# Performance work log

Measured on AMD Instinct MI355X. Metric: run time of the kernel, lower is better.

The kernel has to match this reference:

```python
import jax, jax.numpy as jnp
import numpy as np

N, L, H, Q = 64, 258, 1024, 256
WINDOW = 16.0
DEV_POW = 128.0  # 2 * (window/2)^2, Luong local-p sigma = D/2


def setup_inputs() -> dict:
    key = jax.random.key(0)
    k1, k2, k3, k4, k5, k6 = jax.random.split(key, 6)
    encoder_outputs = jax.random.normal(k1, (N, L, H), dtype=jnp.float32)
    decoder_h_t = jax.random.normal(k2, (N, Q, H), dtype=jnp.float32)
    src_len = jax.random.randint(k3, (N,), 32, L + 1).astype(jnp.int32)
    # window centers within each source sentence
    p_t = jax.random.uniform(k4, (N,), dtype=jnp.float32) * (src_len.astype(jnp.float32) - 1.0)
    W_a = jax.random.normal(k5, (H, H), dtype=jnp.float32) * (1.0 / np.sqrt(H))
    W_c = jax.random.normal(k6, (H, 2 * H), dtype=jnp.float32) * (1.0 / np.sqrt(2 * H))
    return {"encoder_outputs": encoder_outputs, "decoder_h_t": decoder_h_t,
            "src_len": src_len, "p_t": p_t, "W_a": W_a, "W_c": W_c}


def reference(encoder_outputs, decoder_h_t, src_len, p_t, W_a, W_c):
    n, l, h = encoder_outputs.shape
    idx = jnp.arange(l, dtype=jnp.float32)  # index_matrix, length == max_length == L

    # local_p window: [p_t - D, p_t + D], clamped to [0, src_len]
    src_end = src_len.astype(jnp.float32)
    attn_start = jnp.maximum(p_t - WINDOW, 0.0)          # [N]
    attn_end = jnp.minimum(p_t + WINDOW, src_end)        # [N]
    mask = (idx[None, :] < attn_start[:, None]) | (idx[None, :] > attn_end[:, None])  # [N,L]

    # Luong 'general' score: h_t^T W_a h_s -> [N,Q,L]
    score = jnp.einsum('nqh,hk,nlk->nql', decoder_h_t, W_a, encoder_outputs)

    score = jnp.where(mask[:, None, :], -1e9, score)
    align = jax.nn.softmax(score, axis=2)                 # [N,Q,L]

    # gaussian reweighting centered at p_t
    gauss = jnp.exp(-((idx[None, :] - p_t[:, None]) ** 2) / DEV_POW)  # [N,L]
    align = align * gauss[:, None, :]

    context = jnp.einsum('nql,nlh->nqh', align, encoder_outputs)      # [N,Q,H]
    cat = jnp.concatenate([context, decoder_h_t], axis=2)             # [N,Q,2H]
    return jnp.tanh(cat @ W_c.T)                                      # [N,Q,H]
```

## Files before the change

### kernel.cpp

```cpp
#include <hip/hip_runtime.h>
#include <hip/hip_bf16.h>
#include <cstdint>

#define DEVINL __device__ __forceinline__

typedef __attribute__((ext_vector_type(8))) short short8;
typedef __attribute__((ext_vector_type(4))) float f32x4;
typedef __attribute__((ext_vector_type(4))) unsigned short u16x4;

static constexpr int NB = 64, LL = 258, HH = 1024, QQ = 256;
static constexpr int WROWS = 33;
static constexpr int MU = 2176;
static constexpr int VTN = 4096;

static constexpr size_t OFF_META = 0;
static constexpr size_t SZ_WE   = (size_t)MU * HH * 2;
static constexpr size_t OFF_WEHI = 1024;
static constexpr size_t OFF_WELO = OFF_WEHI + SZ_WE;
static constexpr size_t OFF_WAHI = OFF_WELO + SZ_WE;
static constexpr size_t OFF_WALO = OFF_WAHI + (size_t)HH * HH * 2;
static constexpr size_t OFF_WCBF = OFF_WALO + (size_t)HH * HH * 2;
static constexpr size_t OFF_HBF  = OFF_WCBF + (size_t)HH * 2 * HH * 2;
static constexpr size_t OFF_U    = OFF_HBF + (size_t)NB * QQ * HH * 2;
static constexpr size_t OFF_UHI  = OFF_U;
static constexpr size_t OFF_ULO  = OFF_U + (size_t)MU * HH * 2;
static constexpr size_t OFF_PHL  = OFF_U + (size_t)MU * HH * 4;
static constexpr size_t OFF_VT   = OFF_PHL + (size_t)NB * QQ * 128 * 2;

DEVINL unsigned short f2bf(float x) {
    union { float f; uint32_t u; } v; v.f = x;
    uint32_t u = v.u;
    uint32_t r = (u + 0x7FFFu + ((u >> 16) & 1u)) >> 16;
    return (unsigned short)r;
}
DEVINL float bf2f(unsigned short b) {
    union { uint32_t u; float f; } v; v.u = ((uint32_t)b) << 16;
    return v.f;
}

template <typename T>
DEVINL void lds_load16(const T* g, T* l) {
    __builtin_amdgcn_global_load_lds(
        (const __attribute__((address_space(1))) void*)g,
        (__attribute__((address_space(3))) void*)l, 16, 0, 0);
}

DEVINL float fast_tanh(float x) {
    float e = __expf(2.0f * x);
    return 1.0f - 2.0f / (e + 1.0f);
}

DEVINL void window_of(float p, int sl, int& ls, int& lc) {
    float se = (float)sl;
    float s = fmaxf(p - 16.0f, 0.0f);
    float e = fminf(p + 16.0f, se);
    ls = (int)ceilf(s);
    int le = (int)floorf(e); if (le > LL - 1) le = LL - 1;
    lc = le - ls + 1;
    if (lc < 0) lc = 0;
    if (lc > WROWS) lc = WROWS;
}

__global__ __launch_bounds__(256) void k_prep(const float* __restrict__ enc,
                                              const float* __restrict__ pt,
                                              const int* __restrict__ slen,
                                              const float* __restrict__ Wa,
                                              const float* __restrict__ Wc,
                                              unsigned short* __restrict__ wehi,
                                              unsigned short* __restrict__ welo,
                                              unsigned short* __restrict__ wahi,
                                              unsigned short* __restrict__ walo,
                                              unsigned short* __restrict__ wcbf) {
    const int b = blockIdx.x, t = threadIdx.x;
    if (b < MU) {
        int r = b;
        const float* src = nullptr;
        bool valid = false;
        if (r < NB * WROWS) {
            int n = r / WROWS, li = r - n * WROWS;
            int ls, lc;
            window_of(pt[n], slen[n], ls, lc);
            if (li < lc) { valid = true; src = enc + ((size_t)n * LL + ls + li) * HH; }
        }
        f32x4 v;
        if (valid) v = ((const f32x4*)src)[t];
        else { v[0] = 0.f; v[1] = 0.f; v[2] = 0.f; v[3] = 0.f; }
        u16x4 h, l;
#pragma unroll
        for (int j = 0; j < 4; ++j) {
            unsigned short hb = f2bf(v[j]);
            h[j] = hb;
            l[j] = f2bf(v[j] - bf2f(hb));
        }
        size_t o = (size_t)r * HH / 4 + t;
        ((u16x4*)wehi)[o] = h;
        ((u16x4*)welo)[o] = l;
    } else if (b < MU + 1024) {
        int i = (b - MU) * 256 + t;
        f32x4 v = ((const f32x4*)Wa)[i];
        u16x4 h, l;
#pragma unroll
        for (int j = 0; j < 4; ++j) {
            unsigned short hb = f2bf(v[j]);
            h[j] = hb;
            l[j] = f2bf(v[j] - bf2f(hb));
        }
        ((u16x4*)wahi)[i] = h;
        ((u16x4*)walo)[i] = l;
    } else {
        int i = (b - MU - 1024) * 256 + t;
        f32x4 v = ((const f32x4*)Wc)[i];
        u16x4 h;
#pragma unroll
        for (int j = 0; j < 4; ++j) h[j] = f2bf(v[j]);
        ((u16x4*)wcbf)[i] = h;
    }
}

__global__ __launch_bounds__(256) void k_wgemm(const unsigned short* __restrict__ wehi,
                                               const unsigned short* __restrict__ welo,
                                               const unsigned short* __restrict__ wahi,
                                               const unsigned short* __restrict__ walo,
                                               const unsigned short* __restrict__ wcbf,
                                               unsigned short* __restrict__ Uhi,
                                               unsigned short* __restrict__ Ulo,
                                               unsigned short* __restrict__ VT) {
    __shared__ unsigned short smem[24576];
    const int tid = threadIdx.x;
    const int bid = blockIdx.x;

    const int w = tid >> 6, lane = tid & 63;
    const int wr = w >> 1, wc = w & 1;
    const int r16 = lane & 15, khalf = lane >> 4, rg = lane >> 4;
    const int srow = tid >> 2;
    const int scol = ((tid & 3) ^ ((tid >> 3) & 3)) * 8;
    const int kslot = (khalf ^ ((r16 >> 1) & 3)) * 8;

    if (bid < 272) {
        const int m0 = (bid >> 3) * 64;
        const int n0 = (bid & 7) * 128;
        f32x4 acc[2][4] = {};

        auto stage = [&](int buf, int kb) {
            lds_load16(wehi + (size_t)(m0 + srow) * HH + kb + scol, &smem[buf * 2048 + tid * 8]);
            lds_load16(welo + (size_t)(m0 + srow) * HH + kb + scol, &smem[4096 + buf * 2048 + tid * 8]);
#pragma unroll
            for (int i = 0; i < 2; ++i) {
                lds_load16(wahi + (size_t)(n0 + i * 64 + srow) * HH + kb + scol,
                           &smem[8192 + buf * 4096 + i * 2048 + tid * 8]);
                lds_load16(walo + (size_t)(n0 + i * 64 + srow) * HH + kb + scol,
                           &smem[16384 + buf * 4096 + i * 2048 + tid * 8]);
            }
        };

        stage(0, 0);
        for (int t = 0; t < 32; ++t) {
            const int buf = t & 1;
            asm volatile("s_waitcnt vmcnt(0)" ::: "memory");
            __builtin_amdgcn_s_barrier();
            short8 ah[2], al[2], bh[4], bl[4];
#pragma unroll
            for (int f = 0; f < 2; ++f) {
                int ai = buf * 2048 + (wr * 32 + f * 16 + r16) * 32 + kslot;
                ah[f] = *(const short8*)&smem[ai];
                al[f] = *(const short8*)&smem[4096 + ai];
            }
#pragma unroll
            for (int nf = 0; nf < 4; ++nf) {
                int bi = buf * 4096 + (wc * 64 + nf * 16 + r16) * 32 + kslot;
                bh[nf] = *(const short8*)&smem[8192 + bi];
                bl[nf] = *(const short8*)&smem[16384 + bi];
            }
            if (t + 1 < 32) stage(buf ^ 1, (t + 1) * 32);
            asm volatile("s_waitcnt lgkmcnt(0)" ::: "memory");
            __builtin_amdgcn_sched_barrier(0);
#pragma unroll
            for (int mf = 0; mf < 2; ++mf)
#pragma unroll
                for (int nf = 0; nf < 4; ++nf) {
                    acc[mf][nf] = __builtin_amdgcn_mfma_f32_16x16x32_bf16(ah[mf], bh[nf], acc[mf][nf], 0, 0, 0);
                    acc[mf][nf] = __builtin_amdgcn_mfma_f32_16x16x32_bf16(ah[mf], bl[nf], acc[mf][nf], 0, 0, 0);
                    acc[mf][nf] = __builtin_amdgcn_mfma_f32_16x16x32_bf16(al[mf], bh[nf], acc[mf][nf], 0, 0, 0);
                }
            __builtin_amdgcn_s_barrier();
        }
#pragma unroll
        for (int mf = 0; mf < 2; ++mf)
#pragma unroll
            for (int nf = 0; nf < 4; ++nf)
#pragma unroll
                for (int r = 0; r < 4; ++r) {
                    int m = m0 + wr * 32 + mf * 16 + rg * 4 + r;
                    int nn = n0 + wc * 64 + nf * 16 + r16;
                    float v = acc[mf][nf][r];
                    unsigned short h = f2bf(v);
                    Uhi[(size_t)m * HH + nn] = h;
                    Ulo[(size_t)m * HH + nn] = f2bf(v - bf2f(h));
                }
    } else {
        const int b2 = bid - 272;
        const int m0 = (b2 / 17) * 64;
        const int n0 = (b2 % 17) * 128;
        f32x4 acc[2][4] = {};

        auto stage = [&](int buf, int kb) {
            lds_load16(wcbf + (size_t)(m0 + srow) * (2 * HH) + kb + scol, &smem[buf * 2048 + tid * 8]);
#pragma unroll
            for (int i = 0; i < 2; ++i) {
                lds_load16(wehi + (size_t)(n0 + i * 64 + srow) * HH + kb + scol,
                           &smem[8192 + buf * 4096 + i * 2048 + tid * 8]);
                lds_load16(welo + (size_t)(n0 + i * 64 + srow) * HH + kb + scol,
                           &smem[16384 + buf * 4096 + i * 2048 + tid * 8]);
            }
        };

        stage(0, 0);
        for (int t = 0; t < 32; ++t) {
            const int buf = t & 1;
            asm volatile("s_waitcnt vmcnt(0)" ::: "memory");
            __builtin_amdgcn_s_barrier();
            short8 af[2], bh[4], bl[4];
#pragma unroll
            for (int f = 0; f < 2; ++f)
                af[f] = *(const short8*)&smem[buf * 2048 + (wr * 32 + f * 16 + r16) * 32 + kslot];
#pragma unroll
            for (int nf = 0; nf < 4; ++nf) {
                int bi = buf * 4096 + (wc * 64 + nf * 16 + r16) * 32 + kslot;
                bh[nf] = *(const short8*)&smem[8192 + bi];
                bl[nf] = *(const short8*)&smem[16384 + bi];
            }
            if (t + 1 < 32) stage(buf ^ 1, (t + 1) * 32);
            asm volatile("s_waitcnt lgkmcnt(0)" ::: "memory");
            __builtin_amdgcn_sched_barrier(0);
#pragma unroll
            for (int mf = 0; mf < 2; ++mf)
#pragma unroll
                for (int nf = 0; nf < 4; ++nf) {
                    acc[mf][nf] = __builtin_amdgcn_mfma_f32_16x16x32_bf16(af[mf], bh[nf], acc[mf][nf], 0, 0, 0);
                    acc[mf][nf] = __builtin_amdgcn_mfma_f32_16x16x32_bf16(af[mf], bl[nf], acc[mf][nf], 0, 0, 0);
                }
            __builtin_amdgcn_s_barrier();
        }
#pragma unroll
        for (int mf = 0; mf < 2; ++mf)
#pragma unroll
            for (int nf = 0; nf < 4; ++nf)
#pragma unroll
                for (int r = 0; r < 4; ++r) {
                    int o = m0 + wr * 32 + mf * 16 + rg * 4 + r;
                    int wrow = n0 + wc * 64 + nf * 16 + r16;
                    int n = wrow / WROWS, li = wrow - n * WROWS;
                    if (n < NB)
                        VT[(size_t)o * VTN + n * 64 + li] = f2bf(acc[mf][nf][r]);
                }
    }
}

__global__ __launch_bounds__(256) void k_attn2(const float* __restrict__ ht,
                                               const unsigned short* __restrict__ Uhi,
                                               const unsigned short* __restrict__ Ulo,
                                               const float* __restrict__ pt,
                                               const int* __restrict__ slen,
                                               unsigned short* __restrict__ Phl,
                                               unsigned short* __restrict__ hbf) {
    __shared__ float sPart[4][32 * 48];
    __shared__ float sScore[32 * 48];

    const int tid = threadIdx.x;
    const int w = tid >> 6, lane = tid & 63;
    const int n = blockIdx.x >> 3, q0 = (blockIdx.x & 7) * 32;
    int ls, lc;
    window_of(pt[n], slen[n], ls, lc);
    const float p = pt[n];
    const int r16 = lane & 15, khalf = lane >> 4, rg = lane >> 4;

    const float* hbase = ht + ((size_t)(n * QQ + q0)) * HH;
    unsigned short* hbbase = hbf + ((size_t)(n * QQ + q0)) * HH;
    const unsigned short* uhbase = Uhi + (size_t)n * WROWS * HH;
    const unsigned short* ulbase = Ulo + (size_t)n * WROWS * HH;

    f32x4 acc[2][3] = {};
#pragma unroll 2
    for (int ks = 0; ks < 8; ++ks) {
        int kcol = w * 256 + ks * 32 + khalf * 8;
        short8 ah[2], al[2];
#pragma unroll
        for (int mf = 0; mf < 2; ++mf) {
            const float* src = hbase + (size_t)(mf * 16 + r16) * HH + kcol;
            f32x4 v0 = *(const f32x4*)src;
            f32x4 v1 = *(const f32x4*)(src + 4);
            float vv[8] = {v0[0], v0[1], v0[2], v0[3], v1[0], v1[1], v1[2], v1[3]};
#pragma unroll
            for (int j = 0; j < 8; ++j) {
                unsigned short hb = f2bf(vv[j]);
                ah[mf][j] = (short)hb;
                al[mf][j] = (short)f2bf(vv[j] - bf2f(hb));
            }
            *(short8*)(hbbase + (size_t)(mf * 16 + r16) * HH + kcol) = ah[mf];
        }
#pragma unroll
        for (int nf = 0; nf < 3; ++nf) {
            size_t uoff = (size_t)(nf * 16 + r16) * HH + kcol;
            short8 bh = *(const short8*)(uhbase + uoff);
            short8 bl = *(const short8*)(ulbase + uoff);
#pragma unroll
            for (int mf = 0; mf < 2; ++mf) {
                acc[mf][nf] = __builtin_amdgcn_mfma_f32_16x16x32_bf16(ah[mf], bh, acc[mf][nf], 0, 0, 0);
                acc[mf][nf] = __builtin_amdgcn_mfma_f32_16x16x32_bf16(ah[mf], bl, acc[mf][nf], 0, 0, 0);
                acc[mf][nf] = __builtin_amdgcn_mfma_f32_16x16x32_bf16(al[mf], bh, acc[mf][nf], 0, 0, 0);
            }
        }
    }
#pragma unroll
    for (int mf = 0; mf < 2; ++mf)
#pragma unroll
        for (int nf = 0; nf < 3; ++nf)
#pragma unroll
            for (int r = 0; r < 4; ++r)
                sPart[w][(mf * 16 + rg * 4 + r) * 48 + nf * 16 + r16] = acc[mf][nf][r];
    __syncthreads();

    {
        int q = tid >> 3, g = tid & 7;
        float sc6[6];
#pragma unroll
        for (int s = 0; s < 6; ++s) {
            int li = g + 8 * s;
            int o = q * 48 + li;
            sc6[s] = sPart[0][o] + sPart[1][o] + sPart[2][o] + sPart[3][o];
        }
        float mx = -1e30f;
#pragma unroll
        for (int s = 0; s < 6; ++s) { int li = g + 8 * s; if (li < lc) mx = fmaxf(mx, sc6[s]); }
        for (int off = 1; off < 8; off <<= 1) mx = fmaxf(mx, __shfl_xor(mx, off, 8));
        float sum = 0.f, ex[6];
#pragma unroll
        for (int s = 0; s < 6; ++s) {
            int li = g + 8 * s;
            float e = (li < lc) ? __expf(sc6[s] - mx) : 0.f;
            ex[s] = e; sum += e;
        }
        for (int off = 1; off < 8; off <<= 1) sum += __shfl_xor(sum, off, 8);
        float inv = 1.0f / sum;
#pragma unroll
        for (int s = 0; s < 6; ++s) {
            int li = g + 8 * s;
            float d = (float)(ls + li) - p;
            float gs = __expf(-(d * d) * (1.0f / 128.0f));
            sScore[q * 48 + li] = ex[s] * inv * gs;
        }
    }
    __syncthreads();

    {
        int row = tid >> 3, c0 = (tid & 7) * 8;
        short8 ph, pl;
#pragma unroll
        for (int j = 0; j < 8; ++j) {
            int c = c0 + j;
            float pv = (c < 48) ? sScore[row * 48 + c] : 0.f;
            unsigned short hb = f2bf(pv);
            ph[j] = (short)hb;
            pl[j] = (short)f2bf(pv - bf2f(hb));
        }
        size_t base = (size_t)(n * QQ + q0 + row) * 128;
        *(short8*)&Phl[base + c0] = ph;
        *(short8*)&Phl[base + 64 + c0] = pl;
    }
}

__global__ __launch_bounds__(256) void k_out_gemm128(
    const unsigned short* __restrict__ Ahf,
    const unsigned short* __restrict__ Bt,
    const unsigned short* __restrict__ Phl,
    const unsigned short* __restrict__ VT,
    float* __restrict__ out) {
    __shared__ unsigned short sA[128 * 64], sB[128 * 64];

    const int tid = threadIdx.x;
    const int wid = tid >> 6, lane = tid & 63;
    const int bid = blockIdx.x;
    const int swz = (bid & 7) * 128 + (bid >> 3);
    const int mt = swz >> 3, nt = swz & 7;
    const int m0 = mt * 128, n0 = nt * 128;
    const int nb = mt >> 1;
    const int wr = wid >> 1, wc = wid & 1;
    const int r16 = lane & 15, kg = lane >> 4;

    const int srow8 = lane >> 3;
    const int kswz = ((lane & 7) ^ srow8) * 8;

    f32x4 acc[4][4] = {};

    for (int t = 0; t < 18; ++t) {
        if (t > 0) __syncthreads();
        if (t < 16) {
            const int kb = t * 64;
#pragma unroll
            for (int i = 0; i < 4; ++i) {
                int row = i * 32 + wid * 8 + srow8;
                lds_load16(Ahf + (size_t)(m0 + row) * HH + kb + kswz,
                           &sA[i * 2048 + wid * 512]);
                lds_load16(Bt + (size_t)(n0 + row) * (2 * HH) + 1024 + kb + kswz,
                           &sB[i * 2048 + wid * 512]);
            }
        } else {
            const int pc = (t - 16) * 64;
#pragma unroll
            for (int i = 0; i < 4; ++i) {
                int row = i * 32 + wid * 8 + srow8;
                lds_load16(Phl + (size_t)(m0 + row) * 128 + pc + kswz,
                           &sA[i * 2048 + wid * 512]);
                lds_load16(VT + (size_t)(n0 + row) * VTN + nb * 64 + kswz,
                           &sB[i * 2048 + wid * 512]);
            }
        }
        asm volatile("s_waitcnt vmcnt(0)" ::: "memory");
        __syncthreads();

        short8 a[4][2];
#pragma unroll
        for (int mq = 0; mq < 4; ++mq)
#pragma unroll
            for (int ks = 0; ks < 2; ++ks)
                a[mq][ks] = *(const short8*)&sA[(wr * 64 + mq * 16 + r16) * 64 +
                                                (((ks * 4 + kg) ^ (r16 & 7)) * 8)];
#pragma unroll
        for (int nq = 0; nq < 4; ++nq) {
            short8 b0 = *(const short8*)&sB[(wc * 64 + nq * 16 + r16) * 64 +
                                            (((0 + kg) ^ (r16 & 7)) * 8)];
            short8 b1 = *(const short8*)&sB[(wc * 64 + nq * 16 + r16) * 64 +
                                            (((4 + kg) ^ (r16 & 7)) * 8)];
#pragma unroll
            for (int mq = 0; mq < 4; ++mq) {
                acc[mq][nq] = __builtin_amdgcn_mfma_f32_16x16x32_bf16(a[mq][0], b0, acc[mq][nq], 0, 0, 0);
                acc[mq][nq] = __builtin_amdgcn_mfma_f32_16x16x32_bf16(a[mq][1], b1, acc[mq][nq], 0, 0, 0);
            }
        }
    }

#pragma unroll
    for (int mq = 0; mq < 4; ++mq)
#pragma unroll
        for (int nq = 0; nq < 4; ++nq) {
            int row = m0 + wr * 64 + mq * 16 + kg * 4;
            int col = n0 + wc * 64 + nq * 16 + r16;
#pragma unroll
            for (int r = 0; r < 4; ++r)
                out[(size_t)(row + r) * HH + col] = fast_tanh(acc[mq][nq][r]);
        }
}

extern "C" void kernel_launch(void* const* d_in, const int* in_sizes, int n_in,
                              void* d_out, int out_size, void* d_ws, size_t ws_size,
                              hipStream_t stream) {
    const float* enc  = (const float*)d_in[0];
    const float* ht   = (const float*)d_in[1];
    const int*   slen = (const int*)d_in[2];
    const float* pt   = (const float*)d_in[3];
    const float* Wa   = (const float*)d_in[4];
    const float* Wc   = (const float*)d_in[5];
    float* out = (float*)d_out;

    char* ws = (char*)d_ws;
    unsigned short* wehi = (unsigned short*)(ws + OFF_WEHI);
    unsigned short* welo = (unsigned short*)(ws + OFF_WELO);
    unsigned short* wahi = (unsigned short*)(ws + OFF_WAHI);
    unsigned short* walo = (unsigned short*)(ws + OFF_WALO);
    unsigned short* wcbf = (unsigned short*)(ws + OFF_WCBF);
    unsigned short* hbf  = (unsigned short*)(ws + OFF_HBF);
    unsigned short* uhi  = (unsigned short*)(ws + OFF_UHI);
    unsigned short* ulo  = (unsigned short*)(ws + OFF_ULO);
    unsigned short* phl  = (unsigned short*)(ws + OFF_PHL);
    unsigned short* vt   = (unsigned short*)(ws + OFF_VT);

    hipLaunchKernelGGL(k_prep, dim3(MU + 1024 + 2048), dim3(256), 0, stream,
                       enc, pt, slen, Wa, Wc, wehi, welo, wahi, walo, wcbf);
    hipLaunchKernelGGL(k_wgemm, dim3(544), dim3(256), 0, stream,
                       wehi, welo, wahi, walo, wcbf, uhi, ulo, vt);
    hipLaunchKernelGGL(k_attn2, dim3(NB * 8), dim3(256), 0, stream,
                       ht, uhi, ulo, pt, slen, phl, hbf);
    hipLaunchKernelGGL(k_out_gemm128, dim3(1024), dim3(256), 0, stream,
                       hbf, wcbf, phl, vt, out);
}
```

Before: 137.7 us.

## Double-buffer LDS in output GEMM with prefetch of next K tile

Result: slower. 141.4 us (+2.7%).

```diff
diff --git a/kernel.cpp b/kernel.cpp
--- a/kernel.cpp
+++ b/kernel.cpp
@@ -375,7 +375,7 @@
     const unsigned short* __restrict__ Phl,
     const unsigned short* __restrict__ VT,
     float* __restrict__ out) {
-    __shared__ unsigned short sA[128 * 64], sB[128 * 64];
+    __shared__ unsigned short sA[2][4096], sB[2][4096];
 
     const int tid = threadIdx.x;
     const int wid = tid >> 6, lane = tid & 63;
@@ -387,56 +387,57 @@
     const int wr = wid >> 1, wc = wid & 1;
     const int r16 = lane & 15, kg = lane >> 4;
 
-    const int srow8 = lane >> 3;
-    const int kswz = ((lane & 7) ^ srow8) * 8;
+    const int srow = tid >> 2;
+    const int scol = ((tid & 3) ^ ((tid >> 3) & 3)) * 8;
+    const int kslot = (kg ^ ((r16 >> 1) & 3)) * 8;
 
     f32x4 acc[4][4] = {};
 
-    for (int t = 0; t < 18; ++t) {
-        if (t > 0) __syncthreads();
-        if (t < 16) {
-            const int kb = t * 64;
-#pragma unroll
-            for (int i = 0; i < 4; ++i) {
-                int row = i * 32 + wid * 8 + srow8;
-                lds_load16(Ahf + (size_t)(m0 + row) * HH + kb + kswz,
-                           &sA[i * 2048 + wid * 512]);
-                lds_load16(Bt + (size_t)(n0 + row) * (2 * HH) + 1024 + kb + kswz,
-                           &sB[i * 2048 + wid * 512]);
+    auto stage = [&](int buf, int t) {
+        if (t < 32) {
+            const int kb = t * 32;
+#pragma unroll
+            for (int i = 0; i < 2; ++i) {
+                lds_load16(Ahf + (size_t)(m0 + i * 64 + srow) * HH + kb + scol,
+                           &sA[buf][i * 2048 + tid * 8]);
+                lds_load16(Bt + (size_t)(n0 + i * 64 + srow) * (2 * HH) + 1024 + kb + scol,
+                           &sB[buf][i * 2048 + tid * 8]);
             }
         } else {
-            const int pc = (t - 16) * 64;
-#pragma unroll
-            for (int i = 0; i < 4; ++i) {
-                int row = i * 32 + wid * 8 + srow8;
-                lds_load16(Phl + (size_t)(m0 + row) * 128 + pc + kswz,
-                           &sA[i * 2048 + wid * 512]);
-                lds_load16(VT + (size_t)(n0 + row) * VTN + nb * 64 + kswz,
-                           &sB[i * 2048 + wid * 512]);
-            }
-        }
+            const int pidx = t - 32;
+            const int pc = pidx * 32;
+            const int vc = nb * 64 + (pidx & 1) * 32;
+#pragma unroll
+            for (int i = 0; i < 2; ++i) {
+                lds_load16(Phl + (size_t)(m0 + i * 64 + srow) * 128 + pc + scol,
+                           &sA[buf][i * 2048 + tid * 8]);
+                lds_load16(VT + (size_t)(n0 + i * 64 + srow) * VTN + vc + scol,
+                           &sB[buf][i * 2048 + tid * 8]);
+            }
+        }
+    };
+
+    stage(0, 0);
+    for (int t = 0; t < 36; ++t) {
+        const int buf = t & 1;
         asm volatile("s_waitcnt vmcnt(0)" ::: "memory");
-        __syncthreads();
-
-        short8 a[4][2];
+        __builtin_amdgcn_s_barrier();
+        short8 a[4], b[4];
 #pragma unroll
         for (int mq = 0; mq < 4; ++mq)
-#pragma unroll
-            for (int ks = 0; ks < 2; ++ks)
-                a[mq][ks] = *(const short8*)&sA[(wr * 64 + mq * 16 + r16) * 64 +
-                                                (((ks * 4 + kg) ^ (r16 & 7)) * 8)];
-#pragma unroll
-        for (int nq = 0; nq < 4; ++nq) {
-            short8 b0 = *(const short8*)&sB[(wc * 64 + nq * 16 + r16) * 64 +
-                                            (((0 + kg) ^ (r16 & 7)) * 8)];
-            short8 b1 = *(const short8*)&sB[(wc * 64 + nq * 16 + r16) * 64 +
-                                            (((4 + kg) ^ (r16 & 7)) * 8)];
-#pragma unroll
-            for (int mq = 0; mq < 4; ++mq) {
-                acc[mq][nq] = __builtin_amdgcn_mfma_f32_16x16x32_bf16(a[mq][0], b0, acc[mq][nq], 0, 0, 0);
-                acc[mq][nq] = __builtin_amdgcn_mfma_f32_16x16x32_bf16(a[mq][1], b1, acc[mq][nq], 0, 0, 0);
-            }
-        }
+            a[mq] = *(const short8*)&sA[buf][(wr * 64 + mq * 16 + r16) * 32 + kslot];
+#pragma unroll
+        for (int nq = 0; nq < 4; ++nq)
+            b[nq] = *(const short8*)&sB[buf][(wc * 64 + nq * 16 + r16) * 32 + kslot];
+        if (t + 1 < 36) stage(buf ^ 1, t + 1);
+        asm volatile("s_waitcnt lgkmcnt(0)" ::: "memory");
+        __builtin_amdgcn_sched_barrier(0);
+#pragma unroll
+        for (int nq = 0; nq < 4; ++nq)
+#pragma unroll
+            for (int mq = 0; mq < 4; ++mq)
+                acc[mq][nq] = __builtin_amdgcn_mfma_f32_16x16x32_bf16(a[mq], b[nq], acc[mq][nq], 0, 0, 0);
+        __builtin_amdgcn_s_barrier();
     }
 
 #pragma unroll
```

## Double-buffer LDS tiles in output GEMM to overlap global loads with MFMA

Applied to the files above, without the earlier changes.

New measurement: 136.7 us, median of 2. No clear change (-0.7%).

```diff
diff --git a/kernel.cpp b/kernel.cpp
--- a/kernel.cpp
+++ b/kernel.cpp
@@ -375,7 +375,7 @@
     const unsigned short* __restrict__ Phl,
     const unsigned short* __restrict__ VT,
     float* __restrict__ out) {
-    __shared__ unsigned short sA[128 * 64], sB[128 * 64];
+    __shared__ unsigned short sA[2][128 * 64], sB[2][128 * 64];
 
     const int tid = threadIdx.x;
     const int wid = tid >> 6, lane = tid & 63;
@@ -392,17 +392,16 @@
 
     f32x4 acc[4][4] = {};
 
-    for (int t = 0; t < 18; ++t) {
-        if (t > 0) __syncthreads();
+    auto stage = [&](int buf, int t) {
         if (t < 16) {
             const int kb = t * 64;
 #pragma unroll
             for (int i = 0; i < 4; ++i) {
                 int row = i * 32 + wid * 8 + srow8;
                 lds_load16(Ahf + (size_t)(m0 + row) * HH + kb + kswz,
-                           &sA[i * 2048 + wid * 512]);
+                           &sA[buf][i * 2048 + wid * 512]);
                 lds_load16(Bt + (size_t)(n0 + row) * (2 * HH) + 1024 + kb + kswz,
-                           &sB[i * 2048 + wid * 512]);
+                           &sB[buf][i * 2048 + wid * 512]);
             }
         } else {
             const int pc = (t - 16) * 64;
@@ -410,33 +409,49 @@
             for (int i = 0; i < 4; ++i) {
                 int row = i * 32 + wid * 8 + srow8;
                 lds_load16(Phl + (size_t)(m0 + row) * 128 + pc + kswz,
-                           &sA[i * 2048 + wid * 512]);
+                           &sA[buf][i * 2048 + wid * 512]);
                 lds_load16(VT + (size_t)(n0 + row) * VTN + nb * 64 + kswz,
-                           &sB[i * 2048 + wid * 512]);
-            }
-        }
-        asm volatile("s_waitcnt vmcnt(0)" ::: "memory");
-        __syncthreads();
+                           &sB[buf][i * 2048 + wid * 512]);
+            }
+        }
+    };
+
+    stage(0, 0);
+    for (int t = 0; t < 18; ++t) {
+        const int buf = t & 1;
+        if (t + 1 < 18) {
+            stage(buf ^ 1, t + 1);
+            asm volatile("s_waitcnt vmcnt(8)" ::: "memory");
+        } else {
+            asm volatile("s_waitcnt vmcnt(0)" ::: "memory");
+        }
+        __builtin_amdgcn_s_barrier();
 
         short8 a[4][2];
 #pragma unroll
         for (int mq = 0; mq < 4; ++mq)
 #pragma unroll
             for (int ks = 0; ks < 2; ++ks)
-                a[mq][ks] = *(const short8*)&sA[(wr * 64 + mq * 16 + r16) * 64 +
-                                                (((ks * 4 + kg) ^ (r16 & 7)) * 8)];
+                a[mq][ks] = *(const short8*)&sA[buf][(wr * 64 + mq * 16 + r16) * 64 +
+                                                     (((ks * 4 + kg) ^ (r16 & 7)) * 8)];
+        short8 b[4][2];
 #pragma unroll
         for (int nq = 0; nq < 4; ++nq) {
-            short8 b0 = *(const short8*)&sB[(wc * 64 + nq * 16 + r16) * 64 +
-                                            (((0 + kg) ^ (r16 & 7)) * 8)];
-            short8 b1 = *(const short8*)&sB[(wc * 64 + nq * 16 + r16) * 64 +
-                                            (((4 + kg) ^ (r16 & 7)) * 8)];
+            b[nq][0] = *(const short8*)&sB[buf][(wc * 64 + nq * 16 + r16) * 64 +
+                                               (((0 + kg) ^ (r16 & 7)) * 8)];
+            b[nq][1] = *(const short8*)&sB[buf][(wc * 64 + nq * 16 + r16) * 64 +
+                                               (((4 + kg) ^ (r16 & 7)) * 8)];
+        }
+        asm volatile("s_waitcnt lgkmcnt(0)" ::: "memory");
+        __builtin_amdgcn_sched_barrier(0);
+#pragma unroll
+        for (int nq = 0; nq < 4; ++nq)
 #pragma unroll
             for (int mq = 0; mq < 4; ++mq) {
-                acc[mq][nq] = __builtin_amdgcn_mfma_f32_16x16x32_bf16(a[mq][0], b0, acc[mq][nq], 0, 0, 0);
-                acc[mq][nq] = __builtin_amdgcn_mfma_f32_16x16x32_bf16(a[mq][1], b1, acc[mq][nq], 0, 0, 0);
-            }
-        }
+                acc[mq][nq] = __builtin_amdgcn_mfma_f32_16x16x32_bf16(a[mq][0], b[nq][0], acc[mq][nq], 0, 0, 0);
+                acc[mq][nq] = __builtin_amdgcn_mfma_f32_16x16x32_bf16(a[mq][1], b[nq][1], acc[mq][nq], 0, 0, 0);
+            }
+        __builtin_amdgcn_s_barrier();
     }
 
 #pragma unroll
```
